# Kernel optimization log

Hardware: AMD Instinct MI355X
Metric: run time of the kernel (lower is better)

## Reference

```python
import jax, jax.numpy as jnp
import numpy as np

N = 1_000_000
F = 64
G = 8          # num_groups
B = 16         # number of point clouds in batch
EPS = 1e-8


def setup_inputs() -> dict:
    key = jax.random.key(0)
    k1, k2 = jax.random.split(key)
    feats = jax.random.normal(k1, (N, F), dtype=jnp.float32)
    batch_ids = jnp.sort(jax.random.randint(k2, (N,), 0, B))
    gamma = jnp.ones((1, F), dtype=jnp.float32)
    beta = jnp.zeros((1, F), dtype=jnp.float32)
    return {"feats": feats, "batch_ids": batch_ids, "gamma": gamma, "beta": beta}


def reference(feats, batch_ids, gamma, beta):
    gs = F // G  # group_size
    # [N, F] -> [N*gs, G]: each row holds one channel-within-group across all groups
    cur = feats.reshape(-1, G)
    ids = jnp.repeat(batch_ids, gs)  # [N*gs]
    counts = jax.ops.segment_sum(jnp.ones_like(ids, dtype=cur.dtype), ids, num_segments=B)
    counts = jnp.maximum(counts, 1.0)[:, None]                # [B, 1]
    means = jax.ops.segment_sum(cur, ids, num_segments=B) / counts   # [B, G]
    m = means[ids]                                            # [N*gs, G]
    var = jax.ops.segment_sum((cur - m) ** 2, ids, num_segments=B) / counts  # [B, G]
    normed = (cur - m) / jnp.sqrt(var[ids] + EPS)             # [N*gs, G]
    out = normed.reshape(-1, F)
    return out * gamma + beta
```

## Files before the change

kernel.cpp:

```cpp
#include <hip/hip_runtime.h>

#define GN_EPS 1e-8f

static constexpr int F     = 64;
static constexpr int G     = 8;
static constexpr int NB    = 16;
static constexpr int BLK   = 256;
static constexpr int GRID  = 2048;
static constexpr int NSLOT = 16;

typedef float f32x4 __attribute__((ext_vector_type(4)));


__global__ void gn_prep(const int* __restrict__ ids, int n, int* __restrict__ off,
                        float* __restrict__ zbuf ) {
    const int t = threadIdx.x;
    for (int i = t; i < 2 * NSLOT * NB * G; i += BLK) zbuf[i] = 0.f;
    if (t < NB + 1) {
        int lo = 0, hi = n;
        while (lo < hi) {
            int mid = (lo + hi) >> 1;
            if (ids[mid] < t) lo = mid + 1; else hi = mid;
        }
        off[t] = lo;
    }
}

__global__ __launch_bounds__(BLK) void gn_stats(
        const float* __restrict__ feats, const int* __restrict__ off_g, int n,
        float* __restrict__ gsum, float* __restrict__ gsq) {
    __shared__ float lsum[NB * G];
    __shared__ float lsq [NB * G];
    __shared__ int   soff[NB + 1];
    const int t = threadIdx.x;
    if (t < NB * G) { lsum[t] = 0.f; lsq[t] = 0.f; }
    if (t < NB + 1) soff[t] = off_g[t];
    __syncthreads();

    const int rpb  = (n + GRID - 1) / GRID;
    const int row0 = (int)blockIdx.x * rpb;
    const int row1 = min(n, row0 + rpb);

    if (row0 < row1) {
        const int quad   = t & 15;
        const int subrow = t >> 4;
        const int lane   = t & 63;
        int b = 0, cur = row0;
        while (cur < row1) {
            while (soff[b + 1] <= cur) ++b;
            const int send = min(row1, soff[b + 1]);
            float s0=0.f,s1=0.f,s2=0.f,s3=0.f,q0=0.f,q1=0.f,q2=0.f,q3=0.f;
            const float* p = feats + (size_t)(cur + subrow) * F + quad * 4;
            int base = cur;
            for (; base + 64 <= send; base += 64, p += 64 * F) {
                const float4 x0 = *reinterpret_cast<const float4*>(p);
                const float4 x1 = *reinterpret_cast<const float4*>(p + 16 * F);
                const float4 x2 = *reinterpret_cast<const float4*>(p + 32 * F);
                const float4 x3 = *reinterpret_cast<const float4*>(p + 48 * F);
                s0 += x0.x; q0 = fmaf(x0.x, x0.x, q0);
                s1 += x0.y; q1 = fmaf(x0.y, x0.y, q1);
                s2 += x0.z; q2 = fmaf(x0.z, x0.z, q2);
                s3 += x0.w; q3 = fmaf(x0.w, x0.w, q3);
                s0 += x1.x; q0 = fmaf(x1.x, x1.x, q0);
                s1 += x1.y; q1 = fmaf(x1.y, x1.y, q1);
                s2 += x1.z; q2 = fmaf(x1.z, x1.z, q2);
                s3 += x1.w; q3 = fmaf(x1.w, x1.w, q3);
                s0 += x2.x; q0 = fmaf(x2.x, x2.x, q0);
                s1 += x2.y; q1 = fmaf(x2.y, x2.y, q1);
                s2 += x2.z; q2 = fmaf(x2.z, x2.z, q2);
                s3 += x2.w; q3 = fmaf(x2.w, x2.w, q3);
                s0 += x3.x; q0 = fmaf(x3.x, x3.x, q0);
                s1 += x3.y; q1 = fmaf(x3.y, x3.y, q1);
                s2 += x3.z; q2 = fmaf(x3.z, x3.z, q2);
                s3 += x3.w; q3 = fmaf(x3.w, x3.w, q3);
            }
            for (; base + 16 <= send; base += 16, p += 16 * F) {
                const float4 x = *reinterpret_cast<const float4*>(p);
                s0 += x.x; q0 = fmaf(x.x, x.x, q0);
                s1 += x.y; q1 = fmaf(x.y, x.y, q1);
                s2 += x.z; q2 = fmaf(x.z, x.z, q2);
                s3 += x.w; q3 = fmaf(x.w, x.w, q3);
            }
            if (base + subrow < send) {
                const float4 x = *reinterpret_cast<const float4*>(p);
                s0 += x.x; q0 = fmaf(x.x, x.x, q0);
                s1 += x.y; q1 = fmaf(x.y, x.y, q1);
                s2 += x.z; q2 = fmaf(x.z, x.z, q2);
                s3 += x.w; q3 = fmaf(x.w, x.w, q3);
            }
            #pragma unroll
            for (int m = 2; m <= 32; m <<= 1) {
                s0 += __shfl_xor(s0, m); s1 += __shfl_xor(s1, m);
                s2 += __shfl_xor(s2, m); s3 += __shfl_xor(s3, m);
                q0 += __shfl_xor(q0, m); q1 += __shfl_xor(q1, m);
                q2 += __shfl_xor(q2, m); q3 += __shfl_xor(q3, m);
            }
            if (lane < 2) {
                float* ps = &lsum[b * G + lane * 4];
                float* pq = &lsq [b * G + lane * 4];
                atomicAdd(ps + 0, s0); atomicAdd(ps + 1, s1);
                atomicAdd(ps + 2, s2); atomicAdd(ps + 3, s3);
                atomicAdd(pq + 0, q0); atomicAdd(pq + 1, q1);
                atomicAdd(pq + 2, q2); atomicAdd(pq + 3, q3);
            }
            cur = send;
        }
    }
    __syncthreads();
    if (t < NB * G) {
        const int slot = (int)blockIdx.x & (NSLOT - 1);
        atomicAdd(&gsum[slot * NB * G + t], lsum[t]);
        atomicAdd(&gsq [slot * NB * G + t], lsq [t]);
    }
}

__global__ __launch_bounds__(BLK) void gn_norm(
        const float* __restrict__ feats, const int* __restrict__ off_g, int n,
        const float* __restrict__ gsum, const float* __restrict__ gsq,
        const float* __restrict__ gamma, const float* __restrict__ beta,
        float* __restrict__ out) {
    __shared__ int soff[NB + 1];
    const int t = threadIdx.x;
    if (t < NB + 1) soff[t] = off_g[t];
    __syncthreads();

    const int rpb  = (n + GRID - 1) / GRID;
    const int row0 = (int)blockIdx.x * rpb;
    const int row1 = min(n, row0 + rpb);
    if (row0 >= row1) return;

    const int quad   = t & 15;
    const int subrow = t >> 4;
    const float4 gm = *reinterpret_cast<const float4*>(gamma + quad * 4);
    const float4 bt = *reinterpret_cast<const float4*>(beta  + quad * 4);

    int b = NB - 1, e = row1;
    while (e > row0) {
        while (soff[b] >= e) --b;
        const int sstart = max(row0, soff[b]);
        f32x4 sm = {0.f, 0.f, 0.f, 0.f}, sq = {0.f, 0.f, 0.f, 0.f};
        #pragma unroll
        for (int k = 0; k < NSLOT; ++k) {
            sm += *reinterpret_cast<const f32x4*>(gsum + k * NB * G + b * G + (quad & 1) * 4);
            sq += *reinterpret_cast<const f32x4*>(gsq  + k * NB * G + b * G + (quad & 1) * 4);
        }
        const float cnt = (float)max((soff[b + 1] - soff[b]) * (F / G), 1);
        const float rc  = 1.0f / cnt;
        f32x4 a, c;
        {
            const float m0 = sm.x * rc, m1 = sm.y * rc, m2 = sm.z * rc, m3 = sm.w * rc;
            const float v0 = fmaxf(sq.x * rc - m0 * m0, 0.f);
            const float v1 = fmaxf(sq.y * rc - m1 * m1, 0.f);
            const float v2 = fmaxf(sq.z * rc - m2 * m2, 0.f);
            const float v3 = fmaxf(sq.w * rc - m3 * m3, 0.f);
            a.x = gm.x / sqrtf(v0 + GN_EPS); a.y = gm.y / sqrtf(v1 + GN_EPS);
            a.z = gm.z / sqrtf(v2 + GN_EPS); a.w = gm.w / sqrtf(v3 + GN_EPS);
            c.x = fmaf(-m0, a.x, bt.x); c.y = fmaf(-m1, a.y, bt.y);
            c.z = fmaf(-m2, a.z, bt.z); c.w = fmaf(-m3, a.w, bt.w);
        }
        int hi = e;
        for (; hi - sstart >= 64; hi -= 64) {
            const float* p  = feats + (size_t)(hi - 64 + subrow) * F + quad * 4;
            float*       po = out   + (size_t)(hi - 64 + subrow) * F + quad * 4;
            const f32x4 x0 = *reinterpret_cast<const f32x4*>(p);
            const f32x4 x1 = *reinterpret_cast<const f32x4*>(p + 16 * F);
            const f32x4 x2 = *reinterpret_cast<const f32x4*>(p + 32 * F);
            const f32x4 x3 = *reinterpret_cast<const f32x4*>(p + 48 * F);
            f32x4 o0, o1, o2, o3;
            o0.x = fmaf(x0.x, a.x, c.x); o0.y = fmaf(x0.y, a.y, c.y);
            o0.z = fmaf(x0.z, a.z, c.z); o0.w = fmaf(x0.w, a.w, c.w);
            o1.x = fmaf(x1.x, a.x, c.x); o1.y = fmaf(x1.y, a.y, c.y);
            o1.z = fmaf(x1.z, a.z, c.z); o1.w = fmaf(x1.w, a.w, c.w);
            o2.x = fmaf(x2.x, a.x, c.x); o2.y = fmaf(x2.y, a.y, c.y);
            o2.z = fmaf(x2.z, a.z, c.z); o2.w = fmaf(x2.w, a.w, c.w);
            o3.x = fmaf(x3.x, a.x, c.x); o3.y = fmaf(x3.y, a.y, c.y);
            o3.z = fmaf(x3.z, a.z, c.z); o3.w = fmaf(x3.w, a.w, c.w);
            __builtin_nontemporal_store(o0, reinterpret_cast<f32x4*>(po));
            __builtin_nontemporal_store(o1, reinterpret_cast<f32x4*>(po + 16 * F));
            __builtin_nontemporal_store(o2, reinterpret_cast<f32x4*>(po + 32 * F));
            __builtin_nontemporal_store(o3, reinterpret_cast<f32x4*>(po + 48 * F));
        }
        for (; hi - sstart >= 16; hi -= 16) {
            const float* p  = feats + (size_t)(hi - 16 + subrow) * F + quad * 4;
            float*       po = out   + (size_t)(hi - 16 + subrow) * F + quad * 4;
            const f32x4 x = *reinterpret_cast<const f32x4*>(p);
            f32x4 o;
            o.x = fmaf(x.x, a.x, c.x); o.y = fmaf(x.y, a.y, c.y);
            o.z = fmaf(x.z, a.z, c.z); o.w = fmaf(x.w, a.w, c.w);
            __builtin_nontemporal_store(o, reinterpret_cast<f32x4*>(po));
        }
        if (sstart + subrow < hi) {
            const float* p  = feats + (size_t)(sstart + subrow) * F + quad * 4;
            float*       po = out   + (size_t)(sstart + subrow) * F + quad * 4;
            const f32x4 x = *reinterpret_cast<const f32x4*>(p);
            f32x4 o;
            o.x = fmaf(x.x, a.x, c.x); o.y = fmaf(x.y, a.y, c.y);
            o.z = fmaf(x.z, a.z, c.z); o.w = fmaf(x.w, a.w, c.w);
            __builtin_nontemporal_store(o, reinterpret_cast<f32x4*>(po));
        }
        e = sstart;
    }
}

extern "C" void kernel_launch(void* const* d_in, const int* in_sizes, int n_in,
                              void* d_out, int out_size, void* d_ws, size_t ws_size,
                              hipStream_t stream) {
    const float* feats = (const float*)d_in[0];
    const int*   ids   = (const int*)  d_in[1];
    const float* gamma = (const float*)d_in[2];
    const float* beta  = (const float*)d_in[3];
    const int n = in_sizes[1];

    float* gsum = (float*)d_ws;
    float* gsq  = gsum + NSLOT * NB * G;
    int*   off  = (int*)(gsq + NSLOT * NB * G);

    gn_prep <<<1, BLK, 0, stream>>>(ids, n, off, gsum);
    gn_stats<<<GRID, BLK, 0, stream>>>(feats, off, n, gsum, gsq);
    gn_norm <<<GRID, BLK, 0, stream>>>(feats, off, n, gsum, gsq, gamma, beta, (float*)d_out);
}
```

Baseline: 131.2 us.

## Fuse prep, stats and normalize into one persistent kernel with grid barrier

Merges the three launches into a single kernel. Each block computes the segment offsets itself, accumulates its partial statistics, then waits at a global atomic barrier before normalizing its own rows. The grid drops to 512 blocks so that all blocks can be resident at once, and the workspace is cleared with a memset. This removes launch gaps and makes it possible for a block's feature rows to still be in cache when the second pass reads them. In exchange it relies on all blocks being co-resident (a deadlock risk otherwise), adds barrier spin time, and repeats the binary search in every block.

```diff
diff --git a/kernel.cpp b/kernel.cpp
--- a/kernel.cpp
+++ b/kernel.cpp
@@ -6,45 +6,41 @@
 static constexpr int G     = 8;
 static constexpr int NB    = 16;
 static constexpr int BLK   = 256;
-static constexpr int GRID  = 2048;
+static constexpr int GRID  = 512;
 static constexpr int NSLOT = 16;
 
 typedef float f32x4 __attribute__((ext_vector_type(4)));
 
 
-__global__ void gn_prep(const int* __restrict__ ids, int n, int* __restrict__ off,
-                        float* __restrict__ zbuf ) {
+__global__ __launch_bounds__(BLK, 2) void gn_fused(
+        const float* __restrict__ feats, const int* __restrict__ ids, int n,
+        float* __restrict__ gsum, float* __restrict__ gsq, int* __restrict__ bar,
+        const float* __restrict__ gamma, const float* __restrict__ beta,
+        float* __restrict__ out) {
+    __shared__ float lsum[NB * G];
+    __shared__ float lsq [NB * G];
+    __shared__ int   soff[NB + 1];
     const int t = threadIdx.x;
-    for (int i = t; i < 2 * NSLOT * NB * G; i += BLK) zbuf[i] = 0.f;
+
     if (t < NB + 1) {
         int lo = 0, hi = n;
         while (lo < hi) {
             int mid = (lo + hi) >> 1;
             if (ids[mid] < t) lo = mid + 1; else hi = mid;
         }
-        off[t] = lo;
-    }
-}
-
-__global__ __launch_bounds__(BLK) void gn_stats(
-        const float* __restrict__ feats, const int* __restrict__ off_g, int n,
-        float* __restrict__ gsum, float* __restrict__ gsq) {
-    __shared__ float lsum[NB * G];
-    __shared__ float lsq [NB * G];
-    __shared__ int   soff[NB + 1];
-    const int t = threadIdx.x;
+        soff[t] = lo;
+    }
     if (t < NB * G) { lsum[t] = 0.f; lsq[t] = 0.f; }
-    if (t < NB + 1) soff[t] = off_g[t];
     __syncthreads();
 
     const int rpb  = (n + GRID - 1) / GRID;
     const int row0 = (int)blockIdx.x * rpb;
     const int row1 = min(n, row0 + rpb);
+    const int quad   = t & 15;
+    const int subrow = t >> 4;
+    const int lane   = t & 63;
 
     if (row0 < row1) {
-        const int quad   = t & 15;
-        const int subrow = t >> 4;
-        const int lane   = t & 63;
         int b = 0, cur = row0;
         while (cur < row1) {
             while (soff[b + 1] <= cur) ++b;
@@ -112,25 +108,17 @@
         atomicAdd(&gsum[slot * NB * G + t], lsum[t]);
         atomicAdd(&gsq [slot * NB * G + t], lsq [t]);
     }
-}
-
-__global__ __launch_bounds__(BLK) void gn_norm(
-        const float* __restrict__ feats, const int* __restrict__ off_g, int n,
-        const float* __restrict__ gsum, const float* __restrict__ gsq,
-        const float* __restrict__ gamma, const float* __restrict__ beta,
-        float* __restrict__ out) {
-    __shared__ int soff[NB + 1];
-    const int t = threadIdx.x;
-    if (t < NB + 1) soff[t] = off_g[t];
-    __syncthreads();
-
-    const int rpb  = (n + GRID - 1) / GRID;
-    const int row0 = (int)blockIdx.x * rpb;
-    const int row1 = min(n, row0 + rpb);
+
+    __syncthreads();
+    if (t == 0) {
+        __threadfence();
+        __hip_atomic_fetch_add(bar, 1, __ATOMIC_RELEASE, __HIP_MEMORY_SCOPE_AGENT);
+        while (__hip_atomic_load(bar, __ATOMIC_ACQUIRE, __HIP_MEMORY_SCOPE_AGENT) < GRID)
+            __builtin_amdgcn_s_sleep(2);
+    }
+    __syncthreads();
+
     if (row0 >= row1) return;
-
-    const int quad   = t & 15;
-    const int subrow = t >> 4;
     const float4 gm = *reinterpret_cast<const float4*>(gamma + quad * 4);
     const float4 bt = *reinterpret_cast<const float4*>(beta  + quad * 4);
 
@@ -141,8 +129,16 @@
         f32x4 sm = {0.f, 0.f, 0.f, 0.f}, sq = {0.f, 0.f, 0.f, 0.f};
         #pragma unroll
         for (int k = 0; k < NSLOT; ++k) {
-            sm += *reinterpret_cast<const f32x4*>(gsum + k * NB * G + b * G + (quad & 1) * 4);
-            sq += *reinterpret_cast<const f32x4*>(gsq  + k * NB * G + b * G + (quad & 1) * 4);
+            const float* ps = gsum + k * NB * G + b * G + (quad & 1) * 4;
+            const float* pq = gsq  + k * NB * G + b * G + (quad & 1) * 4;
+            sm.x += __hip_atomic_load(ps + 0, __ATOMIC_RELAXED, __HIP_MEMORY_SCOPE_AGENT);
+            sm.y += __hip_atomic_load(ps + 1, __ATOMIC_RELAXED, __HIP_MEMORY_SCOPE_AGENT);
+            sm.z += __hip_atomic_load(ps + 2, __ATOMIC_RELAXED, __HIP_MEMORY_SCOPE_AGENT);
+            sm.w += __hip_atomic_load(ps + 3, __ATOMIC_RELAXED, __HIP_MEMORY_SCOPE_AGENT);
+            sq.x += __hip_atomic_load(pq + 0, __ATOMIC_RELAXED, __HIP_MEMORY_SCOPE_AGENT);
+            sq.y += __hip_atomic_load(pq + 1, __ATOMIC_RELAXED, __HIP_MEMORY_SCOPE_AGENT);
+            sq.z += __hip_atomic_load(pq + 2, __ATOMIC_RELAXED, __HIP_MEMORY_SCOPE_AGENT);
+            sq.w += __hip_atomic_load(pq + 3, __ATOMIC_RELAXED, __HIP_MEMORY_SCOPE_AGENT);
         }
         const float cnt = (float)max((soff[b + 1] - soff[b]) * (F / G), 1);
         const float rc  = 1.0f / cnt;
@@ -213,9 +209,9 @@
 
     float* gsum = (float*)d_ws;
     float* gsq  = gsum + NSLOT * NB * G;
-    int*   off  = (int*)(gsq + NSLOT * NB * G);
-
-    gn_prep <<<1, BLK, 0, stream>>>(ids, n, off, gsum);
-    gn_stats<<<GRID, BLK, 0, stream>>>(feats, off, n, gsum, gsq);
-    gn_norm <<<GRID, BLK, 0, stream>>>(feats, off, n, gsum, gsq, gamma, beta, (float*)d_out);
+    int*   bar  = (int*)(gsq + NSLOT * NB * G);
+
+    hipMemsetAsync(d_ws, 0, (2 * NSLOT * NB * G) * sizeof(float) + sizeof(int), stream);
+    gn_fused<<<GRID, BLK, 0, stream>>>(feats, ids, n, gsum, gsq, bar,
+                                       gamma, beta, (float*)d_out);
 }
```

After: 188.9 us. 44.0% more time.
